# Kernel tuning notes

Hardware: AMD Instinct MI355X
Metric: run time of the kernel (lower is better)

The kernel has to match this reference:

```python
import jax, jax.numpy as jnp
import numpy as np

N_NODES = 150000
D = 64
N_EDGES = 2000000  # bidirectional: 2 * num_train_edges


def setup_inputs() -> dict:
    key = jax.random.key(0)
    k1, k2, k3, k4, k5 = jax.random.split(key, 5)
    nodes_emb = jax.random.normal(k1, (N_NODES, D), dtype=jnp.float32)
    src = jax.random.randint(k2, (N_EDGES,), 0, N_NODES, dtype=jnp.int64 if jax.config.jax_enable_x64 else jnp.int32).astype(jnp.int32)
    dst = jax.random.randint(k3, (N_EDGES,), 0, N_NODES, dtype=jnp.int32)
    W1 = jax.random.normal(k4, (2 * D, D), dtype=jnp.float32) * (1.0 / np.sqrt(2 * D))
    b1 = jnp.zeros((D,), dtype=jnp.float32)
    W2 = jax.random.normal(k5, (D, 1), dtype=jnp.float32) * (1.0 / np.sqrt(D))
    b2 = jnp.zeros((1,), dtype=jnp.float32)
    return {"nodes_emb": nodes_emb, "src": src, "dst": dst,
            "W1": W1, "b1": b1, "W2": W2, "b2": b2}


def reference(nodes_emb, src, dst, W1, b1, W2, b2):
    # Gather per-edge endpoint embeddings and concat: [E, 2D]
    emb_src = nodes_emb[src]          # [E, D]
    emb_dst = nodes_emb[dst]          # [E, D]
    edge_emb = jnp.concatenate([emb_src, emb_dst], axis=1)  # [E, 2D]
    # 2-layer MLP edge scorer: Linear(2D->D) -> ReLU -> Linear(D->1)
    h = jax.nn.relu(edge_emb @ W1 + b1)  # [E, D]
    edge_logits = h @ W2 + b2            # [E, 1]
    return edge_logits
```

## Files before the change

kernel.cpp:

```cpp
#include <hip/hip_runtime.h>

typedef __attribute__((ext_vector_type(8))) short bf16x8;
typedef __attribute__((ext_vector_type(4))) float f32x4;
typedef __attribute__((ext_vector_type(2))) unsigned int u32x2;
typedef __attribute__((ext_vector_type(4))) unsigned int u32x4;

#define LDSTR 136
#define TPW 8

static __device__ __forceinline__ unsigned int pack2bf(float x, float y) {
  unsigned int ux = __builtin_bit_cast(unsigned int, x);
  ux += 0x7fffu + ((ux >> 16) & 1u);
  unsigned int uy = __builtin_bit_cast(unsigned int, y);
  uy += 0x7fffu + ((uy >> 16) & 1u);
  return (ux >> 16) | (uy & 0xffff0000u);
}
static __device__ __forceinline__ unsigned short f2bf_s(float x) {
  unsigned int ux = __builtin_bit_cast(unsigned int, x);
  ux += 0x7fffu + ((ux >> 16) & 1u);
  return (unsigned short)(ux >> 16);
}
static __device__ __forceinline__ bf16x8 make_afrag(float4 lo, float4 hi) {
  u32x4 p;
  p[0] = pack2bf(lo.x, lo.y);
  p[1] = pack2bf(lo.z, lo.w);
  p[2] = pack2bf(hi.x, hi.y);
  p[3] = pack2bf(hi.z, hi.w);
  return __builtin_bit_cast(bf16x8, p);
}

__global__ __launch_bounds__(256) void node_proj(
    const float* __restrict__ emb,
    const float* __restrict__ W1,
    u32x2* __restrict__ P,
    u32x2* __restrict__ Q,
    int N, int ntiles)
{
  __shared__ unsigned short ls_w1t[64 * LDSTR];
  const int tid  = threadIdx.x;
  const int wave = tid >> 6;
  const int lane = tid & 63;
  const int l15  = lane & 15;
  const int quad = lane >> 4;

  for (int i = tid; i < 64 * 128; i += 256) {
    int k = i >> 6, n = i & 63;
    ls_w1t[n * LDSTR + k] = f2bf_s(W1[i]);
  }
  __syncthreads();

  bf16x8 bfragP[4][2], bfragQ[4][2];
  #pragma unroll
  for (int tn = 0; tn < 4; ++tn)
    #pragma unroll
    for (int s = 0; s < 2; ++s) {
      bfragP[tn][s] = *(const bf16x8*)&ls_w1t[(tn * 16 + l15) * LDSTR + s * 32 + quad * 8];
      bfragQ[tn][s] = *(const bf16x8*)&ls_w1t[(tn * 16 + l15) * LDSTR + 64 + s * 32 + quad * 8];
    }

  for (int tile = blockIdx.x * 4 + wave; tile < ntiles; tile += gridDim.x * 4) {
    const int base = tile * 16;

    bf16x8 afr0, afr1;
    {
      int node = base + l15;
      node = (node < N) ? node : N - 1;
      const float* rp = emb + (long long)node * 64 + quad * 8;
      afr0 = make_afrag(*(const float4*)(rp),      *(const float4*)(rp + 4));
      afr1 = make_afrag(*(const float4*)(rp + 32), *(const float4*)(rp + 36));
    }

    f32x4 aP[4], aQ[4];
    #pragma unroll
    for (int tn = 0; tn < 4; ++tn) { aP[tn] = (f32x4){0,0,0,0}; aQ[tn] = (f32x4){0,0,0,0}; }
    #pragma unroll
    for (int tn = 0; tn < 4; ++tn) {
      aP[tn] = __builtin_amdgcn_mfma_f32_16x16x32_bf16(afr0, bfragP[tn][0], aP[tn], 0, 0, 0);
      aQ[tn] = __builtin_amdgcn_mfma_f32_16x16x32_bf16(afr0, bfragQ[tn][0], aQ[tn], 0, 0, 0);
      aP[tn] = __builtin_amdgcn_mfma_f32_16x16x32_bf16(afr1, bfragP[tn][1], aP[tn], 0, 0, 0);
      aQ[tn] = __builtin_amdgcn_mfma_f32_16x16x32_bf16(afr1, bfragQ[tn][1], aQ[tn], 0, 0, 0);
    }

    #pragma unroll
    for (int r = 0; r < 4; ++r) {
      const int m = base + quad * 4 + r;
      if (m < N) {
        u32x2 vp, vq;
        vp[0] = pack2bf(aP[0][r], aP[1][r]);
        vp[1] = pack2bf(aP[2][r], aP[3][r]);
        vq[0] = pack2bf(aQ[0][r], aQ[1][r]);
        vq[1] = pack2bf(aQ[2][r], aQ[3][r]);
        P[(long long)m * 16 + l15] = vp;
        Q[(long long)m * 16 + l15] = vq;
      }
    }
  }
}

__global__ __launch_bounds__(256) void edge_score(
    const unsigned short* __restrict__ P,
    const unsigned short* __restrict__ Q,
    const int*   __restrict__ src,
    const int*   __restrict__ dst,
    const float* __restrict__ b1,
    const float* __restrict__ W2,
    const float* __restrict__ b2,
    float*       __restrict__ out,
    int E)
{
  const int tid  = blockIdx.x * 256 + threadIdx.x;
  const int lane = threadIdx.x & 63;
  const int s    = lane & 7;
  const int g    = lane >> 3;
  const int wid  = tid >> 6;
  const int nwav = gridDim.x * 4;

  float b1v[8], w2v[8];
  #pragma unroll
  for (int j = 0; j < 8; ++j) {
    const int pos = s * 8 + j;
    const int ch  = (pos & 3) * 16 + (pos >> 2);
    b1v[j] = b1[ch];
    w2v[j] = W2[ch];
  }
  const float b2v = b2[0];
  const int so16 = s * 8;

#define DOT8(PV, QV, ACC)                                                     \
  {                                                                           \
    u32x4 pu = __builtin_bit_cast(u32x4, PV);                                 \
    u32x4 qu = __builtin_bit_cast(u32x4, QV);                                 \
    _Pragma("unroll")                                                         \
    for (int i = 0; i < 4; ++i) {                                             \
      float pl = __builtin_bit_cast(float, pu[i] << 16);                      \
      float ph = __builtin_bit_cast(float, pu[i] & 0xffff0000u);              \
      float ql = __builtin_bit_cast(float, qu[i] << 16);                      \
      float qh = __builtin_bit_cast(float, qu[i] & 0xffff0000u);              \
      float h0 = fmaxf(pl + ql + b1v[2 * i], 0.f);                            \
      float h1 = fmaxf(ph + qh + b1v[2 * i + 1], 0.f);                        \
      ACC = __builtin_fmaf(h0, w2v[2 * i], ACC);                              \
      ACC = __builtin_fmaf(h1, w2v[2 * i + 1], ACC);                          \
    }                                                                         \
  }

  const int step = nwav * 16;
  for (int e0 = wid * 16; e0 < E; e0 += step) {
    int eA = e0 + g;
    int eB = e0 + 8 + g;
    const int eAc = (eA < E) ? eA : (E - 1);
    const int eBc = (eB < E) ? eB : (E - 1);
    const int siA = src[eAc], diA = dst[eAc];
    const int siB = src[eBc], diB = dst[eBc];

    const bf16x8 pvA = *(const bf16x8*)(P + (long long)siA * 64 + so16);
    const bf16x8 qvA = *(const bf16x8*)(Q + (long long)diA * 64 + so16);
    const bf16x8 pvB = *(const bf16x8*)(P + (long long)siB * 64 + so16);
    const bf16x8 qvB = *(const bf16x8*)(Q + (long long)diB * 64 + so16);

    float accA = 0.f, accB = 0.f;
    DOT8(pvA, qvA, accA);
    DOT8(pvB, qvB, accB);

    accA += __shfl_xor(accA, 1); accB += __shfl_xor(accB, 1);
    accA += __shfl_xor(accA, 2); accB += __shfl_xor(accB, 2);
    accA += __shfl_xor(accA, 4); accB += __shfl_xor(accB, 4);

    if (s == 0) {
      if (eA < E) out[eA] = accA + b2v;
      if (eB < E) out[eB] = accB + b2v;
    }
  }
#undef DOT8
}

__global__ __launch_bounds__(256) void edge_mlp_f32(
    const float* __restrict__ nodes_emb, const int* __restrict__ src,
    const int* __restrict__ dst, const float* __restrict__ W1,
    const float* __restrict__ b1, const float* __restrict__ W2,
    const float* __restrict__ b2, float* __restrict__ out, int E)
{
  __shared__ unsigned short ls_w1t[64 * LDSTR];
  __shared__ float ls_b1[64];
  __shared__ float ls_w2[64];
  const int tid = threadIdx.x, wave = tid >> 6, lane = tid & 63;
  const int l15 = lane & 15, quad = lane >> 4;
  for (int i = tid; i < 64 * 128; i += 256) {
    int n = i >> 7, k = i & 127;
    ls_w1t[n * LDSTR + k] = f2bf_s(W1[k * 64 + n]);
  }
  if (tid < 64) { ls_b1[tid] = b1[tid]; ls_w2[tid] = W2[tid]; }
  __syncthreads();
  bf16x8 bfrag[4][4];
  #pragma unroll
  for (int tn = 0; tn < 4; ++tn)
    #pragma unroll
    for (int s = 0; s < 4; ++s)
      bfrag[tn][s] = *(const bf16x8*)&ls_w1t[(tn * 16 + l15) * LDSTR + s * 32 + quad * 8];
  float myb1[4], myw2[4];
  #pragma unroll
  for (int tn = 0; tn < 4; ++tn) { myb1[tn] = ls_b1[tn*16+l15]; myw2[tn] = ls_w2[tn*16+l15]; }
  const float b2v = b2[0];
  const int wave_base = blockIdx.x * (TPW * 64) + wave * (TPW * 16);
  #pragma unroll 1
  for (int t = 0; t < TPW; ++t) {
    const int tile_base = wave_base + t * 16;
    if (tile_base >= E) break;
    const int e = tile_base + l15;
    const int si = src[e], di = dst[e];
    const float* srow = nodes_emb + (long long)si * 64 + quad * 8;
    const float* drow = nodes_emb + (long long)di * 64 + quad * 8;
    float4 v0 = *(const float4*)(srow),      v1 = *(const float4*)(srow + 4);
    float4 v2 = *(const float4*)(srow + 32), v3 = *(const float4*)(srow + 36);
    float4 v4 = *(const float4*)(drow),      v5 = *(const float4*)(drow + 4);
    float4 v6 = *(const float4*)(drow + 32), v7 = *(const float4*)(drow + 36);
    bf16x8 afr[4] = {make_afrag(v0,v1), make_afrag(v2,v3), make_afrag(v4,v5), make_afrag(v6,v7)};
    f32x4 acc[4];
    #pragma unroll
    for (int tn = 0; tn < 4; ++tn) acc[tn] = (f32x4){0.f,0.f,0.f,0.f};
    #pragma unroll
    for (int s = 0; s < 4; ++s)
      #pragma unroll
      for (int tn = 0; tn < 4; ++tn)
        acc[tn] = __builtin_amdgcn_mfma_f32_16x16x32_bf16(afr[s], bfrag[tn][s], acc[tn], 0, 0, 0);
    #pragma unroll
    for (int r = 0; r < 4; ++r) {
      float p = 0.f;
      #pragma unroll
      for (int tn = 0; tn < 4; ++tn) {
        float h = fmaxf(acc[tn][r] + myb1[tn], 0.f);
        p = __builtin_fmaf(h, myw2[tn], p);
      }
      p += __shfl_xor(p, 1); p += __shfl_xor(p, 2);
      p += __shfl_xor(p, 4); p += __shfl_xor(p, 8);
      if (l15 == 0) out[tile_base + quad * 4 + r] = p + b2v;
    }
  }
}

extern "C" void kernel_launch(void* const* d_in, const int* in_sizes, int n_in,
                              void* d_out, int out_size, void* d_ws, size_t ws_size,
                              hipStream_t stream) {
  const float* nodes_emb = (const float*)d_in[0];
  const int*   src       = (const int*)d_in[1];
  const int*   dst       = (const int*)d_in[2];
  const float* W1        = (const float*)d_in[3];
  const float* b1        = (const float*)d_in[4];
  const float* W2        = (const float*)d_in[5];
  const float* b2        = (const float*)d_in[6];
  float* out = (float*)d_out;

  const int E = in_sizes[1];
  const int nodes_elems = in_sizes[0];
  const int N = nodes_elems / 64;
  const size_t szP = (size_t)nodes_elems * 2;
  const size_t need = szP * 2;

  if (ws_size >= need) {
    u32x2* P = (u32x2*)d_ws;
    u32x2* Q = (u32x2*)((char*)d_ws + szP);
    const int ntiles = (N + 15) / 16;
    hipLaunchKernelGGL(node_proj, dim3(512), dim3(256), 0, stream,
                       nodes_emb, W1, P, Q, N, ntiles);
    hipLaunchKernelGGL(edge_score, dim3(2048), dim3(256), 0, stream,
                       (const unsigned short*)P, (const unsigned short*)Q,
                       src, dst, b1, W2, b2, out, E);
  } else {
    const int epb = TPW * 64;
    const int blocks = (E + epb - 1) / epb;
    hipLaunchKernelGGL(edge_mlp_f32, dim3(blocks), dim3(256), 0, stream,
                       nodes_emb, src, dst, W1, b1, W2, b2, out, E);
  }
}
```

Baseline: 173.7 us.

## Fold b1 into node projection and process four edge groups per wave iteration

Bias b1 is now added to P during the per-node projection, so the edge kernel no longer loads or adds it for each edge. The edge kernel handles four groups of 8 edges per loop iteration instead of two, which puts more independent gathers in flight per wave. Both kernels also launch twice as many blocks. The cost is higher register pressure in edge_score, and rounding b1 into the bf16 P values slightly changes the numerics.

New measurement: 176.3 us. No clear change (+1.5%).

```diff
diff --git a/kernel.cpp b/kernel.cpp
--- a/kernel.cpp
+++ b/kernel.cpp
@@ -32,6 +32,7 @@
 __global__ __launch_bounds__(256) void node_proj(
     const float* __restrict__ emb,
     const float* __restrict__ W1,
+    const float* __restrict__ b1,
     u32x2* __restrict__ P,
     u32x2* __restrict__ Q,
     int N, int ntiles)
@@ -50,13 +51,16 @@
   __syncthreads();
 
   bf16x8 bfragP[4][2], bfragQ[4][2];
-  #pragma unroll
-  for (int tn = 0; tn < 4; ++tn)
+  float myb1[4];
+  #pragma unroll
+  for (int tn = 0; tn < 4; ++tn) {
+    myb1[tn] = b1[tn * 16 + l15];
     #pragma unroll
     for (int s = 0; s < 2; ++s) {
       bfragP[tn][s] = *(const bf16x8*)&ls_w1t[(tn * 16 + l15) * LDSTR + s * 32 + quad * 8];
       bfragQ[tn][s] = *(const bf16x8*)&ls_w1t[(tn * 16 + l15) * LDSTR + 64 + s * 32 + quad * 8];
     }
+  }
 
   for (int tile = blockIdx.x * 4 + wave; tile < ntiles; tile += gridDim.x * 4) {
     const int base = tile * 16;
@@ -86,8 +90,8 @@
       const int m = base + quad * 4 + r;
       if (m < N) {
         u32x2 vp, vq;
-        vp[0] = pack2bf(aP[0][r], aP[1][r]);
-        vp[1] = pack2bf(aP[2][r], aP[3][r]);
+        vp[0] = pack2bf(aP[0][r] + myb1[0], aP[1][r] + myb1[1]);
+        vp[1] = pack2bf(aP[2][r] + myb1[2], aP[3][r] + myb1[3]);
         vq[0] = pack2bf(aQ[0][r], aQ[1][r]);
         vq[1] = pack2bf(aQ[2][r], aQ[3][r]);
         P[(long long)m * 16 + l15] = vp;
@@ -102,7 +106,6 @@
     const unsigned short* __restrict__ Q,
     const int*   __restrict__ src,
     const int*   __restrict__ dst,
-    const float* __restrict__ b1,
     const float* __restrict__ W2,
     const float* __restrict__ b2,
     float*       __restrict__ out,
@@ -115,12 +118,11 @@
   const int wid  = tid >> 6;
   const int nwav = gridDim.x * 4;
 
-  float b1v[8], w2v[8];
+  float w2v[8];
   #pragma unroll
   for (int j = 0; j < 8; ++j) {
     const int pos = s * 8 + j;
     const int ch  = (pos & 3) * 16 + (pos >> 2);
-    b1v[j] = b1[ch];
     w2v[j] = W2[ch];
   }
   const float b2v = b2[0];
@@ -136,38 +138,55 @@
       float ph = __builtin_bit_cast(float, pu[i] & 0xffff0000u);              \
       float ql = __builtin_bit_cast(float, qu[i] << 16);                      \
       float qh = __builtin_bit_cast(float, qu[i] & 0xffff0000u);              \
-      float h0 = fmaxf(pl + ql + b1v[2 * i], 0.f);                            \
-      float h1 = fmaxf(ph + qh + b1v[2 * i + 1], 0.f);                        \
+      float h0 = fmaxf(pl + ql, 0.f);                                         \
+      float h1 = fmaxf(ph + qh, 0.f);                                         \
       ACC = __builtin_fmaf(h0, w2v[2 * i], ACC);                              \
       ACC = __builtin_fmaf(h1, w2v[2 * i + 1], ACC);                          \
     }                                                                         \
   }
 
-  const int step = nwav * 16;
-  for (int e0 = wid * 16; e0 < E; e0 += step) {
-    int eA = e0 + g;
-    int eB = e0 + 8 + g;
+  const int step = nwav * 32;
+  for (int e0 = wid * 32; e0 < E; e0 += step) {
+    const int eA = e0 + g;
+    const int eB = e0 + 8 + g;
+    const int eC = e0 + 16 + g;
+    const int eD = e0 + 24 + g;
     const int eAc = (eA < E) ? eA : (E - 1);
     const int eBc = (eB < E) ? eB : (E - 1);
+    const int eCc = (eC < E) ? eC : (E - 1);
+    const int eDc = (eD < E) ? eD : (E - 1);
     const int siA = src[eAc], diA = dst[eAc];
     const int siB = src[eBc], diB = dst[eBc];
+    const int siC = src[eCc], diC = dst[eCc];
+    const int siD = src[eDc], diD = dst[eDc];
 
     const bf16x8 pvA = *(const bf16x8*)(P + (long long)siA * 64 + so16);
     const bf16x8 qvA = *(const bf16x8*)(Q + (long long)diA * 64 + so16);
     const bf16x8 pvB = *(const bf16x8*)(P + (long long)siB * 64 + so16);
     const bf16x8 qvB = *(const bf16x8*)(Q + (long long)diB * 64 + so16);
-
-    float accA = 0.f, accB = 0.f;
+    const bf16x8 pvC = *(const bf16x8*)(P + (long long)siC * 64 + so16);
+    const bf16x8 qvC = *(const bf16x8*)(Q + (long long)diC * 64 + so16);
+    const bf16x8 pvD = *(const bf16x8*)(P + (long long)siD * 64 + so16);
+    const bf16x8 qvD = *(const bf16x8*)(Q + (long long)diD * 64 + so16);
+
+    float accA = 0.f, accB = 0.f, accC = 0.f, accD = 0.f;
     DOT8(pvA, qvA, accA);
     DOT8(pvB, qvB, accB);
+    DOT8(pvC, qvC, accC);
+    DOT8(pvD, qvD, accD);
 
     accA += __shfl_xor(accA, 1); accB += __shfl_xor(accB, 1);
+    accC += __shfl_xor(accC, 1); accD += __shfl_xor(accD, 1);
     accA += __shfl_xor(accA, 2); accB += __shfl_xor(accB, 2);
+    accC += __shfl_xor(accC, 2); accD += __shfl_xor(accD, 2);
     accA += __shfl_xor(accA, 4); accB += __shfl_xor(accB, 4);
+    accC += __shfl_xor(accC, 4); accD += __shfl_xor(accD, 4);
 
     if (s == 0) {
       if (eA < E) out[eA] = accA + b2v;
       if (eB < E) out[eB] = accB + b2v;
+      if (eC < E) out[eC] = accC + b2v;
+      if (eD < E) out[eD] = accD + b2v;
     }
   }
 #undef DOT8
@@ -259,11 +278,11 @@
     u32x2* P = (u32x2*)d_ws;
     u32x2* Q = (u32x2*)((char*)d_ws + szP);
     const int ntiles = (N + 15) / 16;
-    hipLaunchKernelGGL(node_proj, dim3(512), dim3(256), 0, stream,
-                       nodes_emb, W1, P, Q, N, ntiles);
-    hipLaunchKernelGGL(edge_score, dim3(2048), dim3(256), 0, stream,
+    hipLaunchKernelGGL(node_proj, dim3(1024), dim3(256), 0, stream,
+                       nodes_emb, W1, b1, P, Q, N, ntiles);
+    hipLaunchKernelGGL(edge_score, dim3(4096), dim3(256), 0, stream,
                        (const unsigned short*)P, (const unsigned short*)Q,
-                       src, dst, b1, W2, b2, out, E);
+                       src, dst, W2, b2, out, E);
   } else {
     const int epb = TPW * 64;
     const int blocks = (E + epb - 1) / epb;
```
